# Kernel tuning notes

Measured on AMD Instinct MI355X. Metric: run time of the kernel, lower is better.

Reference implementation:

```python
import jax, jax.numpy as jnp
import numpy as np

NUM_HEADS = 16
DIM = 1024
HD = DIM // NUM_HEADS  # 64


def setup_inputs() -> dict:
    key = jax.random.key(0)
    ks = jax.random.split(key, 7)
    B, S = 4, 2048
    def xavier(k, shape, fan_in, fan_out):
        bound = float(np.sqrt(6.0 / (fan_in + fan_out)))
        return jax.random.uniform(k, shape, jnp.float32, -bound, bound)
    return {
        "q": jax.random.normal(ks[0], (B, S, DIM), jnp.float32),
        "k": jax.random.normal(ks[1], (B, S, DIM), jnp.float32),
        "v": jax.random.normal(ks[2], (B, S, DIM), jnp.float32),
        "Wq": xavier(ks[3], (NUM_HEADS, DIM, HD), DIM, HD),
        "Wk": xavier(ks[4], (NUM_HEADS, DIM, HD), DIM, HD),
        "Wv": xavier(ks[5], (NUM_HEADS, DIM, HD), DIM, HD),
        "Wo": xavier(ks[6], (DIM, DIM), DIM, DIM),
    }


def reference(q, k, v, Wq, Wk, Wv, Wo):
    B, S, D = q.shape
    norm = jnp.sqrt(jnp.asarray(HD, q.dtype))
    # per-head projections: [B,S,D] x [H,D,hd] -> [B,H,S,hd]
    qh = jnp.einsum('bsd,hde->bhse', q, Wq)
    kh = jnp.einsum('bsd,hde->bhse', k, Wk)
    vh = jnp.einsum('bsd,hde->bhse', v, Wv)
    # scores [B,H,S,S]
    scores = jnp.einsum('bhse,bhte->bhst', qh, kh) / norm
    causal = jnp.triu(jnp.ones((S, S), bool), k=1)
    scores = jnp.where(causal, -jnp.inf, scores)
    attn = jax.nn.softmax(scores, axis=-1)
    out = jnp.einsum('bhst,bhte->bhse', attn, vh)  # [B,H,S,hd]
    # faithful to original: a raw view of [B,H,S,hd] -> [B,S,H*hd] (no head transpose)
    out = out.reshape(B, S, NUM_HEADS * HD)
    return jnp.matmul(out, Wo)
```

## Files before the change

### kernel.cpp

```cpp
#include <hip/hip_runtime.h>
#include <hip/hip_bf16.h>
#include <stdint.h>

typedef __bf16 bf16;
typedef __bf16 bf16x8 __attribute__((ext_vector_type(8)));
typedef __bf16 bf16x4 __attribute__((ext_vector_type(4)));
typedef __bf16 bf16x2 __attribute__((ext_vector_type(2)));
typedef float f32x4 __attribute__((ext_vector_type(4)));
typedef float f32x16 __attribute__((ext_vector_type(16)));
typedef int i32x4 __attribute__((ext_vector_type(4)));

#define NH   16
#define SEQ  2048
#define DM   1024
#define HD   64

__device__ __forceinline__ int swz(int r, int o) {
  return o ^ ((r & 7) << 4) ^ (((r >> 3) & 1) << 5);
}

__device__ __forceinline__ void gll16(const void* g, void* l) {
  __builtin_amdgcn_global_load_lds(
      (__attribute__((address_space(1))) unsigned int*)(g),
      (__attribute__((address_space(3))) unsigned int*)(l), 16, 0, 0);
}

__device__ __forceinline__ int pk2(float a, float b) {
  bf16x2 t; t[0] = (bf16)a; t[1] = (bf16)b;
  return __builtin_bit_cast(int, t);
}

__global__ __launch_bounds__(256) void conv_wt(const float* __restrict__ Wq,
                                               const float* __restrict__ Wk,
                                               const float* __restrict__ Wv,
                                               const float* __restrict__ Wo,
                                               bf16* __restrict__ WqT,
                                               bf16* __restrict__ WkT,
                                               bf16* __restrict__ WvT,
                                               bf16* __restrict__ WoT) {
  __shared__ float tile[64][65];
  int z = blockIdx.z, t = threadIdx.x;
  int d0 = blockIdx.x << 6;
  if (z < 3) {
    const float* W = (z == 0 ? Wq : z == 1 ? Wk : Wv) + ((size_t)blockIdx.y << 16);
#pragma unroll
    for (int i = 0; i < 4; ++i) {
      int slot = (i << 8) + t;
      int r = slot >> 4, c4 = (slot & 15) << 2;
      float4 fv = *(const float4*)(W + (size_t)(d0 + r) * 64 + c4);
      tile[r][c4] = fv.x; tile[r][c4 + 1] = fv.y;
      tile[r][c4 + 2] = fv.z; tile[r][c4 + 3] = fv.w;
    }
  } else {
    int n0 = blockIdx.y << 6;
#pragma unroll
    for (int i = 0; i < 4; ++i) {
      int slot = (i << 8) + t;
      int r = slot >> 4, c4 = (slot & 15) << 2;
      float4 fv = *(const float4*)(Wo + (size_t)(d0 + r) * 1024 + n0 + c4);
      tile[r][c4] = fv.x; tile[r][c4 + 1] = fv.y;
      tile[r][c4 + 2] = fv.z; tile[r][c4 + 3] = fv.w;
    }
  }
  __syncthreads();
  bf16* Wt = z == 0 ? WqT : z == 1 ? WkT : z == 2 ? WvT : WoT;
  size_t base = (z < 3) ? ((size_t)blockIdx.y << 16)
                        : (size_t)(blockIdx.y << 6) * 1024;
  int e = t >> 2, dq = (t & 3) << 4;
  bf16x8 o0, o1;
#pragma unroll
  for (int j = 0; j < 8; ++j) {
    o0[j] = (bf16)tile[dq + j][e];
    o1[j] = (bf16)tile[dq + 8 + j][e];
  }
  bf16* p = Wt + base + (size_t)e * 1024 + d0 + dq;
  *(bf16x8*)p = o0;
  *(bf16x8*)(p + 8) = o1;
}

__global__ __launch_bounds__(256) void conv_in(const float* __restrict__ q,
                                               const float* __restrict__ k,
                                               const float* __restrict__ v,
                                               bf16* __restrict__ qb,
                                               bf16* __restrict__ kb,
                                               bf16* __restrict__ vb) {
  int z = blockIdx.y;
  const float* src = z == 0 ? q : z == 1 ? k : v;
  bf16* dst = z == 0 ? qb : z == 1 ? kb : vb;
  int i = (blockIdx.x * 256 + threadIdx.x) << 3;
  float4 f0 = *(const float4*)(src + i);
  float4 f1 = *(const float4*)(src + i + 4);
  bf16x8 o;
  o[0] = (bf16)f0.x; o[1] = (bf16)f0.y; o[2] = (bf16)f0.z; o[3] = (bf16)f0.w;
  o[4] = (bf16)f1.x; o[5] = (bf16)f1.y; o[6] = (bf16)f1.z; o[7] = (bf16)f1.w;
  *(bf16x8*)(dst + i) = o;
}

template <bool AF32>
__device__ __forceinline__ void gemm_body(char* sm, const void* Av,
                                          const bf16* Bt, void* Cv, int epi,
                                          float scale, int n0, int m0) {
  char* As = sm;
  char* Bs = sm + 16384;
  int tid = threadIdx.x;
  int wid = tid >> 6, lane = tid & 63;
  int g = lane >> 4, cc = lane & 15;
  int wr = wid >> 1, wc = wid & 1;

  f32x4 acc[4][4];
#pragma unroll
  for (int a = 0; a < 4; ++a)
#pragma unroll
    for (int b = 0; b < 4; ++b)
#pragma unroll
      for (int j = 0; j < 4; ++j) acc[a][b][j] = 0.0f;

  for (int kt = 0; kt < 16; ++kt) {
    int k0 = kt << 6;
#pragma unroll
    for (int it = 0; it < 4; ++it) {
      int L = (it << 12) + (tid << 4);
      int r = L >> 7, o = L & 127;
      int os = swz(r, o);
      gll16(Bt + (size_t)(n0 + r) * 1024 + k0 + (os >> 1),
            Bs + (it << 12) + (wid << 10));
    }
    if constexpr (AF32) {
      const float* A = (const float*)Av;
      int r = tid >> 1, hf = tid & 1;
      const float* src = A + (size_t)(m0 + r) * 1024 + k0 + hf * 32;
      float4 fv[8];
#pragma unroll
      for (int q = 0; q < 8; ++q) fv[q] = ((const float4*)src)[q];
#pragma unroll
      for (int q = 0; q < 4; ++q) {
        float4 a = fv[2 * q], b = fv[2 * q + 1];
        bf16x8 pk;
        pk[0] = (bf16)a.x; pk[1] = (bf16)a.y; pk[2] = (bf16)a.z; pk[3] = (bf16)a.w;
        pk[4] = (bf16)b.x; pk[5] = (bf16)b.y; pk[6] = (bf16)b.z; pk[7] = (bf16)b.w;
        *(bf16x8*)(As + (r << 7) + swz(r, hf * 64 + q * 16)) = pk;
      }
    } else {
      const bf16* A = (const bf16*)Av;
#pragma unroll
      for (int it = 0; it < 4; ++it) {
        int L = (it << 12) + (tid << 4);
        int r = L >> 7, o = L & 127;
        int os = swz(r, o);
        gll16(A + (size_t)(m0 + r) * 1024 + k0 + (os >> 1),
              As + (it << 12) + (wid << 10));
      }
    }
    __syncthreads();
#pragma unroll
    for (int kk = 0; kk < 2; ++kk) {
      bf16x8 af[4], bfr[4];
#pragma unroll
      for (int fm = 0; fm < 4; ++fm) {
        int r = (wr << 6) + (fm << 4) + cc;
        af[fm] = *(const bf16x8*)(As + (r << 7) + swz(r, (kk << 6) + (g << 4)));
      }
#pragma unroll
      for (int fn = 0; fn < 4; ++fn) {
        int r = (wc << 6) + (fn << 4) + cc;
        bfr[fn] = *(const bf16x8*)(Bs + (r << 7) + swz(r, (kk << 6) + (g << 4)));
      }
#pragma unroll
      for (int fm = 0; fm < 4; ++fm)
#pragma unroll
        for (int fn = 0; fn < 4; ++fn)
          acc[fm][fn] = __builtin_amdgcn_mfma_f32_16x16x32_bf16(
              af[fm], bfr[fn], acc[fm][fn], 0, 0, 0);
    }
    __syncthreads();
  }

#pragma unroll
  for (int fm = 0; fm < 4; ++fm) {
#pragma unroll
    for (int fn = 0; fn < 4; ++fn) {
      f32x4 v = acc[fm][fn];
      int mr = m0 + (wr << 6) + (fm << 4) + (g << 2);
      int n = n0 + (wc << 6) + (fn << 4) + cc;
      if (epi == 2) {
        float* C = (float*)Cv;
#pragma unroll
        for (int j = 0; j < 4; ++j) C[(size_t)(mr + j) * 1024 + n] = v[j];
      } else if (epi == 0) {
        bf16* C = (bf16*)Cv;
        int h = n >> 6, e = n & 63;
#pragma unroll
        for (int j = 0; j < 4; ++j) {
          int b = (mr + j) >> 11, s = (mr + j) & 2047;
          C[((size_t)(b * NH + h) * SEQ + s) * HD + e] = (bf16)(v[j] * scale);
        }
      } else {
        bf16* C = (bf16*)Cv;
        int h = n >> 6, e = n & 63;
        int b = mr >> 11, s = mr & 2047;
        bf16x4 t;
#pragma unroll
        for (int j = 0; j < 4; ++j) t[j] = (bf16)v[j];
        *(bf16x4*)(C + ((size_t)(b * NH + h) * HD + e) * SEQ + s) = t;
      }
    }
  }
}

__global__ __launch_bounds__(256, 4) void gemm_qkv_bf16(
    const bf16* __restrict__ qb, const bf16* __restrict__ kb,
    const bf16* __restrict__ vb, const bf16* __restrict__ Wq,
    const bf16* __restrict__ Wk, const bf16* __restrict__ Wv,
    bf16* __restrict__ Qh, bf16* __restrict__ Kh, bf16* __restrict__ Vt,
    float qscale) {
  __shared__ char sm[32768];
  int z = blockIdx.z;
  const void* A = z == 0 ? (const void*)qb : z == 1 ? (const void*)kb : (const void*)vb;
  const bf16* B = z == 0 ? Wq : z == 1 ? Wk : Wv;
  void* C = z == 0 ? (void*)Qh : z == 1 ? (void*)Kh : (void*)Vt;
  gemm_body<false>(sm, A, B, C, z == 2 ? 1 : 0, z == 0 ? qscale : 1.0f,
                   (int)blockIdx.x << 7, (int)blockIdx.y << 7);
}

__global__ __launch_bounds__(256, 2) void gemm_qkv_f32(
    const float* __restrict__ q, const float* __restrict__ k,
    const float* __restrict__ v, const bf16* __restrict__ Wq,
    const bf16* __restrict__ Wk, const bf16* __restrict__ Wv,
    bf16* __restrict__ Qh, bf16* __restrict__ Kh, bf16* __restrict__ Vt,
    float qscale) {
  __shared__ char sm[32768];
  int z = blockIdx.z;
  const void* A = z == 0 ? (const void*)q : z == 1 ? (const void*)k : (const void*)v;
  const bf16* B = z == 0 ? Wq : z == 1 ? Wk : Wv;
  void* C = z == 0 ? (void*)Qh : z == 1 ? (void*)Kh : (void*)Vt;
  gemm_body<true>(sm, A, B, C, z == 2 ? 1 : 0, z == 0 ? qscale : 1.0f,
                  (int)blockIdx.x << 7, (int)blockIdx.y << 7);
}

__global__ __launch_bounds__(256, 4) void gemm_o(const bf16* __restrict__ Att,
                                                 const bf16* __restrict__ Wo,
                                                 float* __restrict__ out) {
  __shared__ char sm[32768];
  gemm_body<false>(sm, Att, Wo, out, 2, 1.0f,
                   (int)blockIdx.x << 7, (int)blockIdx.y << 7);
}

__global__ __launch_bounds__(128, 2) void attn_fwd(const bf16* __restrict__ Qh,
                                                   const bf16* __restrict__ Kh,
                                                   const bf16* __restrict__ Vt,
                                                   bf16* __restrict__ Oa) {
  __shared__ char sm[32768];
  int tid = threadIdx.x, wid = tid >> 6;
  int lane = tid & 63, cc = lane & 31, hi = lane >> 5;
  int h4 = hi << 2;
  int bx = blockIdx.x, by = blockIdx.y;
  int bh = (bx << 3) + (by >> 4);
  int pr = by & 15;
  const bf16* Kb = Kh + (size_t)bh * SEQ * HD;
  const bf16* Vb = Vt + (size_t)bh * HD * SEQ;

  bf16x8 vones;
#pragma unroll
  for (int j = 0; j < 8; ++j) vones[j] = (bf16)1.0f;

  for (int ph = 0; ph < 2; ++ph) {
    int qx = ph ? (31 - pr) : pr;
    int q0 = qx << 6;
    int sb = q0 + (wid << 5);

    const bf16* Qp = Qh + ((size_t)bh * SEQ + sb + cc) * HD + (hi << 3);
    bf16x8 qf[4];
#pragma unroll
    for (int kk = 0; kk < 4; ++kk) qf[kk] = *(const bf16x8*)(Qp + (kk << 4));

    f32x16 acc[2], lac;
#pragma unroll
    for (int eb = 0; eb < 2; ++eb)
#pragma unroll
      for (int r = 0; r < 16; ++r) acc[eb][r] = 0.f;
#pragma unroll
    for (int r = 0; r < 16; ++r) lac[r] = 0.f;

    int nkv = qx + 1;
    int cur = 0;
#pragma unroll
    for (int i2 = 0; i2 < 4; ++i2) {
      int L = (i2 << 11) + (tid << 4);
      int r = L >> 7, o = L & 127;
      int os = swz(r, o);
      gll16(Kb + (size_t)r * HD + (os >> 1),
            sm + (i2 << 11) + (wid << 10));
      gll16(Vb + (size_t)r * SEQ + (os >> 1),
            sm + 8192 + (i2 << 11) + (wid << 10));
    }
    asm volatile("s_waitcnt vmcnt(0)" ::: "memory");
    __builtin_amdgcn_s_barrier();
    __builtin_amdgcn_sched_barrier(0);

    for (int it = 0; it < nkv; ++it) {
      int t0 = it << 6;
      char* Ks = sm + (cur << 14);
      char* Vs = Ks + 8192;
      if (it + 1 < nkv) {
        char* nb = sm + ((cur ^ 1) << 14);
        int t1 = t0 + 64;
#pragma unroll
        for (int i2 = 0; i2 < 4; ++i2) {
          int L = (i2 << 11) + (tid << 4);
          int r = L >> 7, o = L & 127;
          int os = swz(r, o);
          gll16(Kb + (size_t)(t1 + r) * HD + (os >> 1),
                nb + (i2 << 11) + (wid << 10));
          gll16(Vb + (size_t)r * SEQ + t1 + (os >> 1),
                nb + 8192 + (i2 << 11) + (wid << 10));
        }
      }
      if (t0 <= sb + 31) {
        f32x16 sc[2];
#pragma unroll
        for (int tb = 0; tb < 2; ++tb) {
#pragma unroll
          for (int r = 0; r < 16; ++r) sc[tb][r] = 0.f;
#pragma unroll
          for (int kk = 0; kk < 4; ++kk) {
            int rr = (tb << 5) + cc;
            bf16x8 kf = *(const bf16x8*)(Ks + (rr << 7) +
                                         swz(rr, (kk << 5) + (hi << 4)));
            sc[tb] = __builtin_amdgcn_mfma_f32_32x32x16_bf16(kf, qf[kk],
                                                             sc[tb], 0, 0, 0);
          }
        }
        if (t0 + 63 > sb) {
          int s = sb + cc;
#pragma unroll
          for (int tb = 0; tb < 2; ++tb)
#pragma unroll
            for (int r = 0; r < 16; ++r) {
              int t = t0 + (tb << 5) + (r & 3) + ((r >> 2) << 3) + h4;
              if (t > s) sc[tb][r] = -3e38f;
            }
        }
#pragma unroll
        for (int tb = 0; tb < 2; ++tb)
#pragma unroll
          for (int r = 0; r < 16; ++r) sc[tb][r] = exp2f(sc[tb][r]);
#pragma unroll
        for (int ks = 0; ks < 4; ++ks) {
          int tb = ks >> 1, base = (ks & 1) << 3;
          int w00 = pk2(sc[tb][base + 0], sc[tb][base + 1]);
          int w01 = pk2(sc[tb][base + 2], sc[tb][base + 3]);
          int w10 = pk2(sc[tb][base + 4], sc[tb][base + 5]);
          int w11 = pk2(sc[tb][base + 6], sc[tb][base + 7]);
          int selB0 = hi ? w00 : w10;
          int selB1 = hi ? w01 : w11;
          int cross0 = __shfl_xor(selB0, 32, 64);
          int cross1 = __shfl_xor(selB1, 32, 64);
          i32x4 wv;
          wv[0] = hi ? cross0 : w00;
          wv[1] = hi ? cross1 : w01;
          wv[2] = hi ? w10 : cross0;
          wv[3] = hi ? w11 : cross1;
          bf16x8 pa = __builtin_bit_cast(bf16x8, wv);
          lac = __builtin_amdgcn_mfma_f32_32x32x16_bf16(pa, vones, lac,
                                                        0, 0, 0);
#pragma unroll
          for (int eb = 0; eb < 2; ++eb) {
            int rr = (eb << 5) + cc;
            bf16x8 vf = *(const bf16x8*)(Vs + (rr << 7) +
                                         swz(rr, (ks << 5) + (hi << 4)));
            acc[eb] = __builtin_amdgcn_mfma_f32_32x32x16_bf16(pa, vf,
                                                              acc[eb], 0, 0, 0);
          }
        }
      }
      asm volatile("s_waitcnt vmcnt(0)" ::: "memory");
      __builtin_amdgcn_s_barrier();
      __builtin_amdgcn_sched_barrier(0);
      cur ^= 1;
    }
    bf16* Op = Oa + ((size_t)bh * SEQ + sb) * HD;
#pragma unroll
    for (int r = 0; r < 16; ++r) {
      float ir = __builtin_amdgcn_rcpf(lac[r]);
      int ssel = (r & 3) + ((r >> 2) << 3) + h4;
#pragma unroll
      for (int eb = 0; eb < 2; ++eb)
        Op[(size_t)ssel * HD + (eb << 5) + cc] = (bf16)(acc[eb][r] * ir);
    }
  }
}

extern "C" void kernel_launch(void* const* d_in, const int* in_sizes, int n_in,
                              void* d_out, int out_size, void* d_ws,
                              size_t ws_size, hipStream_t stream) {
  const float* q = (const float*)d_in[0];
  const float* k = (const float*)d_in[1];
  const float* v = (const float*)d_in[2];
  const float* Wq = (const float*)d_in[3];
  const float* Wk = (const float*)d_in[4];
  const float* Wv = (const float*)d_in[5];
  const float* Wo = (const float*)d_in[6];
  char* ws = (char*)d_ws;

  const size_t MB = 1024 * 1024;
  const float qscale = 0.125f * 1.44269504f;

  bf16* WqT = (bf16*)(ws + 0 * MB);
  bf16* WkT = (bf16*)(ws + 2 * MB);
  bf16* WvT = (bf16*)(ws + 4 * MB);
  bf16* WoT = (bf16*)(ws + 6 * MB);

  conv_wt<<<dim3(16, 16, 4), 256, 0, stream>>>(Wq, Wk, Wv, Wo,
                                               WqT, WkT, WvT, WoT);

  if (ws_size >= 104 * MB) {
    bf16* qb = (bf16*)(ws + 8 * MB);
    bf16* kb = (bf16*)(ws + 24 * MB);
    bf16* vb = (bf16*)(ws + 40 * MB);
    bf16* Qh = (bf16*)(ws + 56 * MB);
    bf16* Kh = (bf16*)(ws + 72 * MB);
    bf16* Vt = (bf16*)(ws + 88 * MB);
    bf16* Att = qb;

    conv_in<<<dim3(4096, 3), 256, 0, stream>>>(q, k, v, qb, kb, vb);
    gemm_qkv_bf16<<<dim3(8, 64, 3), 256, 0, stream>>>(
        qb, kb, vb, WqT, WkT, WvT, Qh, Kh, Vt, qscale);
    attn_fwd<<<dim3(8, 128), 128, 0, stream>>>(Qh, Kh, Vt, Att);
    gemm_o<<<dim3(8, 64), 256, 0, stream>>>(Att, WoT, (float*)d_out);
  } else {
    bf16* Qh = (bf16*)(ws + 8 * MB);
    bf16* Kh = (bf16*)(ws + 24 * MB);
    bf16* Vt = (bf16*)(ws + 40 * MB);
    bf16* Att = (bf16*)(ws + 56 * MB);

    gemm_qkv_f32<<<dim3(8, 64, 3), 256, 0, stream>>>(
        q, k, v, WqT, WkT, WvT, Qh, Kh, Vt, qscale);
    attn_fwd<<<dim3(8, 128), 128, 0, stream>>>(Qh, Kh, Vt, Att);
    gemm_o<<<dim3(8, 64), 256, 0, stream>>>(Att, WoT, (float*)d_out);
  }
}
```

Baseline: 201.4 us.

## Permute K rows on load to drop cross-lane shuffles in attention P packing

K rows are loaded into shared memory in a permuted order (bits 2 and 3 of the row index swapped). The score MFMA output then lands in the register order the PV MFMA's A operand expects, so the per-step __shfl_xor exchanges and selects are removed. The causal-mask index formula is adjusted to match. Separately, the fp32-to-bf16 input conversion kernel now handles 16 elements per thread with half as many blocks. The main risk is getting the permutation consistent with the mask and the V layout.

```diff
diff --git a/kernel.cpp b/kernel.cpp
--- a/kernel.cpp
+++ b/kernel.cpp
@@ -17,6 +17,10 @@
 
 __device__ __forceinline__ int swz(int r, int o) {
   return o ^ ((r & 7) << 4) ^ (((r >> 3) & 1) << 5);
+}
+
+__device__ __forceinline__ int tauK(int m) {
+  return (m & ~12) | ((m & 4) << 1) | ((m & 8) >> 1);
 }
 
 __device__ __forceinline__ void gll16(const void* g, void* l) {
@@ -87,13 +91,18 @@
   int z = blockIdx.y;
   const float* src = z == 0 ? q : z == 1 ? k : v;
   bf16* dst = z == 0 ? qb : z == 1 ? kb : vb;
-  int i = (blockIdx.x * 256 + threadIdx.x) << 3;
+  int i = (blockIdx.x * 256 + threadIdx.x) << 4;
   float4 f0 = *(const float4*)(src + i);
   float4 f1 = *(const float4*)(src + i + 4);
-  bf16x8 o;
-  o[0] = (bf16)f0.x; o[1] = (bf16)f0.y; o[2] = (bf16)f0.z; o[3] = (bf16)f0.w;
-  o[4] = (bf16)f1.x; o[5] = (bf16)f1.y; o[6] = (bf16)f1.z; o[7] = (bf16)f1.w;
-  *(bf16x8*)(dst + i) = o;
+  float4 f2 = *(const float4*)(src + i + 8);
+  float4 f3 = *(const float4*)(src + i + 12);
+  bf16x8 o0, o1;
+  o0[0] = (bf16)f0.x; o0[1] = (bf16)f0.y; o0[2] = (bf16)f0.z; o0[3] = (bf16)f0.w;
+  o0[4] = (bf16)f1.x; o0[5] = (bf16)f1.y; o0[6] = (bf16)f1.z; o0[7] = (bf16)f1.w;
+  o1[0] = (bf16)f2.x; o1[1] = (bf16)f2.y; o1[2] = (bf16)f2.z; o1[3] = (bf16)f2.w;
+  o1[4] = (bf16)f3.x; o1[5] = (bf16)f3.y; o1[6] = (bf16)f3.z; o1[7] = (bf16)f3.w;
+  *(bf16x8*)(dst + i) = o0;
+  *(bf16x8*)(dst + i + 8) = o1;
 }
 
 template <bool AF32>
@@ -252,7 +261,6 @@
   __shared__ char sm[32768];
   int tid = threadIdx.x, wid = tid >> 6;
   int lane = tid & 63, cc = lane & 31, hi = lane >> 5;
-  int h4 = hi << 2;
   int bx = blockIdx.x, by = blockIdx.y;
   int bh = (bx << 3) + (by >> 4);
   int pr = by & 15;
@@ -288,7 +296,7 @@
       int L = (i2 << 11) + (tid << 4);
       int r = L >> 7, o = L & 127;
       int os = swz(r, o);
-      gll16(Kb + (size_t)r * HD + (os >> 1),
+      gll16(Kb + (size_t)tauK(r) * HD + (os >> 1),
             sm + (i2 << 11) + (wid << 10));
       gll16(Vb + (size_t)r * SEQ + (os >> 1),
             sm + 8192 + (i2 << 11) + (wid << 10));
@@ -309,7 +317,7 @@
           int L = (i2 << 11) + (tid << 4);
           int r = L >> 7, o = L & 127;
           int os = swz(r, o);
-          gll16(Kb + (size_t)(t1 + r) * HD + (os >> 1),
+          gll16(Kb + (size_t)(t1 + tauK(r)) * HD + (os >> 1),
                 nb + (i2 << 11) + (wid << 10));
           gll16(Vb + (size_t)r * SEQ + t1 + (os >> 1),
                 nb + 8192 + (i2 << 11) + (wid << 10));
@@ -336,7 +344,8 @@
           for (int tb = 0; tb < 2; ++tb)
 #pragma unroll
             for (int r = 0; r < 16; ++r) {
-              int t = t0 + (tb << 5) + (r & 3) + ((r >> 2) << 3) + h4;
+              int t = t0 + (tb << 5) + (r & 3) + (((r >> 2) & 1) << 2) +
+                      (hi << 3) + ((r >> 3) << 4);
               if (t > s) sc[tb][r] = -3e38f;
             }
         }
@@ -347,19 +356,11 @@
 #pragma unroll
         for (int ks = 0; ks < 4; ++ks) {
           int tb = ks >> 1, base = (ks & 1) << 3;
-          int w00 = pk2(sc[tb][base + 0], sc[tb][base + 1]);
-          int w01 = pk2(sc[tb][base + 2], sc[tb][base + 3]);
-          int w10 = pk2(sc[tb][base + 4], sc[tb][base + 5]);
-          int w11 = pk2(sc[tb][base + 6], sc[tb][base + 7]);
-          int selB0 = hi ? w00 : w10;
-          int selB1 = hi ? w01 : w11;
-          int cross0 = __shfl_xor(selB0, 32, 64);
-          int cross1 = __shfl_xor(selB1, 32, 64);
           i32x4 wv;
-          wv[0] = hi ? cross0 : w00;
-          wv[1] = hi ? cross1 : w01;
-          wv[2] = hi ? w10 : cross0;
-          wv[3] = hi ? w11 : cross1;
+          wv[0] = pk2(sc[tb][base + 0], sc[tb][base + 1]);
+          wv[1] = pk2(sc[tb][base + 2], sc[tb][base + 3]);
+          wv[2] = pk2(sc[tb][base + 4], sc[tb][base + 5]);
+          wv[3] = pk2(sc[tb][base + 6], sc[tb][base + 7]);
           bf16x8 pa = __builtin_bit_cast(bf16x8, wv);
           lac = __builtin_amdgcn_mfma_f32_32x32x16_bf16(pa, vones, lac,
                                                         0, 0, 0);
@@ -382,7 +383,7 @@
 #pragma unroll
     for (int r = 0; r < 16; ++r) {
       float ir = __builtin_amdgcn_rcpf(lac[r]);
-      int ssel = (r & 3) + ((r >> 2) << 3) + h4;
+      int ssel = (r & 3) + ((r >> 2) << 3) + (hi << 2);
 #pragma unroll
       for (int eb = 0; eb < 2; ++eb)
         Op[(size_t)ssel * HD + (eb << 5) + cc] = (bf16)(acc[eb][r] * ir);
@@ -422,7 +423,7 @@
     bf16* Vt = (bf16*)(ws + 88 * MB);
     bf16* Att = qb;
 
-    conv_in<<<dim3(4096, 3), 256, 0, stream>>>(q, k, v, qb, kb, vb);
+    conv_in<<<dim3(2048, 3), 256, 0, stream>>>(q, k, v, qb, kb, vb);
     gemm_qkv_bf16<<<dim3(8, 64, 3), 256, 0, stream>>>(
         qb, kb, vb, WqT, WkT, WvT, Qh, Kh, Vt, qscale);
     attn_fwd<<<dim3(8, 128), 128, 0, stream>>>(Qh, Kh, Vt, Att);
```

Result: faster. 193.4 us (-4.0%).
